# Kernel tuning notes

Hardware: AMD Instinct MI355X
Metric: run time of the kernel (lower is better)

The kernel has to match this reference:

```python
import jax, jax.numpy as jnp
import numpy as np

N_NODES = 100000
N_EDGES = 1280000
D_IN = 64
D_HID = 128
D_OUT = 64


def sage_conv(x, src, dst, W_l, b_l, W_r, n_nodes):
    # PyG SAGEConv (aggr='mean', root_weight=True):
    #   out_i = W_l @ mean_{j in N(i)} x_j + b_l + W_r @ x_i
    msg = x[src]  # [E, d] gather of source-node features
    agg = jax.ops.segment_sum(msg, dst, num_segments=n_nodes)  # [N, d]
    cnt = jax.ops.segment_sum(jnp.ones((src.shape[0], 1), x.dtype), dst,
                              num_segments=n_nodes)  # [N, 1]
    mean = agg / jnp.maximum(cnt, 1.0)  # zero-neighbor nodes -> 0 (matches scatter-mean)
    return mean @ W_l.T + b_l + x @ W_r.T


def setup_inputs() -> dict:
    key = jax.random.key(0)
    ks = jax.random.split(key, 8)
    x = jax.random.normal(ks[0], (N_NODES, D_IN), dtype=jnp.float32)
    edge_index = jax.random.randint(ks[1], (2, N_EDGES), 0, N_NODES, dtype=jnp.int64)
    s = 0.05
    W_l1 = jax.random.normal(ks[2], (D_HID, D_IN), dtype=jnp.float32) * s
    b_l1 = jnp.zeros((D_HID,), dtype=jnp.float32)
    W_r1 = jax.random.normal(ks[3], (D_HID, D_IN), dtype=jnp.float32) * s
    W_l2 = jax.random.normal(ks[4], (D_OUT, D_HID), dtype=jnp.float32) * s
    b_l2 = jnp.zeros((D_OUT,), dtype=jnp.float32)
    W_r2 = jax.random.normal(ks[5], (D_OUT, D_HID), dtype=jnp.float32) * s
    return {"x": x, "edge_index": edge_index,
            "W_l1": W_l1, "b_l1": b_l1, "W_r1": W_r1,
            "W_l2": W_l2, "b_l2": b_l2, "W_r2": W_r2}


def reference(x, edge_index, W_l1, b_l1, W_r1, W_l2, b_l2, W_r2):
    src, dst = edge_index[0], edge_index[1]
    n = x.shape[0]
    h = sage_conv(x, src, dst, W_l1, b_l1, W_r1, n)
    h = jax.nn.relu(h)
    out = sage_conv(h, src, dst, W_l2, b_l2, W_r2, n)
    return out
```

## Files before the change

### kernel.cpp

```cpp
#include <hip/hip_runtime.h>
#include <cstdint>
#include <cstddef>

typedef __attribute__((ext_vector_type(8))) short short8;
typedef __attribute__((ext_vector_type(4))) float floatx4;
typedef __attribute__((ext_vector_type(2))) float floatx2;
typedef __attribute__((ext_vector_type(4))) int intx4;

static constexpr int DIN  = 64;
static constexpr int DHID = 128;
static constexpr int BSH  = 7;
static constexpr int BNODES = 1 << BSH;
static constexpr int TILE = 8192;
static constexpr int CAP  = 4096;
static constexpr unsigned SENT = 0xFFFFFFFFu;

__device__ inline short f2bf(float f) {
  unsigned u = __float_as_uint(f);
  u += 0x7FFF + ((u >> 16) & 1);
  return (short)(u >> 16);
}
__device__ inline float bf2f(short s) {
  return __uint_as_float(((unsigned)(unsigned short)s) << 16);
}
__device__ inline floatx2 bfpair(unsigned u) {
  floatx2 r;
  r[0] = __uint_as_float(u << 16);
  r[1] = __uint_as_float(u & 0xFFFF0000u);
  return r;
}

__global__ __launch_bounds__(256) void part_prep_kernel(const void* edges, long long nmax,
    int* __restrict__ bucket_cursor, int* __restrict__ real_cnt,
    unsigned* __restrict__ packed, int E, int NB,
    const float* __restrict__ x,
    const float* __restrict__ Wl1, const float* __restrict__ Wr1,
    const float* __restrict__ Wl2, const float* __restrict__ Wr2,
    short* __restrict__ xb, short* __restrict__ wc1, short* __restrict__ wc2,
    int nx, int gP, int gx)
{
  __shared__ unsigned sval[TILE];
  __shared__ unsigned saux[TILE];
  __shared__ int hist[1024];
  __shared__ int gb[1024];
  __shared__ int smode;
  int t = threadIdx.x;
  int blk = blockIdx.x;
  if (blk >= gP) {
    int b = blk - gP;
    if (b < gx) {
      int i0 = (b * 256 + t) * 8;
      if (i0 < nx) {
        floatx4 f0 = *(const floatx4*)&x[i0];
        floatx4 f1 = *(const floatx4*)&x[i0 + 4];
        short8 o;
        o[0]=f2bf(f0[0]); o[1]=f2bf(f0[1]); o[2]=f2bf(f0[2]); o[3]=f2bf(f0[3]);
        o[4]=f2bf(f1[0]); o[5]=f2bf(f1[1]); o[6]=f2bf(f1[2]); o[7]=f2bf(f1[3]);
        *(short8*)&xb[i0] = o;
      }
    } else {
      int wb = b - gx;
      int idx = ((wb & 15) * 256 + t) * 4;
      int n = idx >> 7, k = idx & 127;
      const float* src;
      if (wb < 16) src = (k < 64) ? &Wl1[n * 64 + k] : &Wr1[n * 64 + (k - 64)];
      else         src = (n < 64) ? &Wl2[n * 128 + k] : &Wr2[(n - 64) * 128 + k];
      floatx4 f = *(const floatx4*)src;
      short* dst = (wb < 16 ? wc1 : wc2) + idx;
      dst[0]=f2bf(f[0]); dst[1]=f2bf(f[1]); dst[2]=f2bf(f[2]); dst[3]=f2bf(f[3]);
    }
    return;
  }
  int base = blk * TILE;
  int cnt_here = E - base; if (cnt_here > TILE) cnt_here = TILE;
  for (int i = t; i < NB; i += 256) hist[i] = 0;
  if (t == 0) smode = 1;
  __syncthreads();
  {
    const long long* e64 = (const long long*)edges;
    int nchk = E < 256 ? E : 256;
    bool ok = true;
    for (int i = t; i < nchk; i += 256) {
      long long v = e64[i];
      if (v < 0 || v >= nmax) ok = false;
    }
    if (!ok) smode = 0;
  }
  __syncthreads();
  bool m64 = (smode != 0);
  #pragma unroll 4
  for (int c = 0; c < TILE / 256; ++c) {
    int idx = c * 256 + t;
    if (idx < cnt_here) {
      int i = base + idx;
      int s, d;
      if (m64) { const long long* e = (const long long*)edges; s = (int)e[i]; d = (int)e[(size_t)E + i]; }
      else     { const int*       e = (const int*)edges;       s = e[i];      d = e[(size_t)E + i]; }
      int b = d >> BSH;
      int rank = atomicAdd(&hist[b], 1);
      sval[idx] = ((unsigned)(d & (BNODES - 1)) << 17) | (unsigned)s;
      saux[idx] = ((unsigned)b << 13) | (unsigned)rank;
    }
  }
  __syncthreads();
  for (int b = t; b < NB; b += 256) {
    int cnt = hist[b];
    int gbase = 0;
    if (cnt > 0) {
      int pad = (cnt + 15) & ~15;
      gbase = b * CAP + atomicAdd(&bucket_cursor[b], pad);
      atomicAdd(&real_cnt[b], cnt);
      for (int j = cnt; j < pad; ++j) packed[gbase + j] = SENT;
    }
    gb[b] = gbase;
  }
  __syncthreads();
  #pragma unroll 4
  for (int c = 0; c < TILE / 256; ++c) {
    int idx = c * 256 + t;
    if (idx < cnt_here) {
      unsigned a = saux[idx];
      packed[gb[a >> 13] + (a & 0x1FFFu)] = sval[idx];
    }
  }
}

__global__ __launch_bounds__(256) void bucket_sort_agg_kernel(const unsigned* __restrict__ packed,
    const int* __restrict__ bucket_cursor, const int* __restrict__ real_cnt,
    int* __restrict__ row_ptr, int* __restrict__ sorted_src,
    const short* __restrict__ feat, short* __restrict__ meanb, int N, int E) {
  __shared__ int nhist[BNODES];
  __shared__ int cur[BNODES];
  __shared__ int begs[BNODES];
  __shared__ int elist[CAP];
  __shared__ int wsum[4];
  __shared__ int redsum[4];
  int b = blockIdx.x, t = threadIdx.x;
  int partial = 0;
  for (int i = t; i < b; i += 256) partial += real_cnt[i];
  #pragma unroll
  for (int off = 1; off < 64; off <<= 1) partial += __shfl_xor(partial, off, 64);
  if ((t & 63) == 0) redsum[t >> 6] = partial;
  if (t < BNODES) nhist[t] = 0;
  if (b == 0 && t == 0) row_ptr[N] = E;
  __syncthreads();
  int eb = redsum[0] + redsum[1] + redsum[2] + redsum[3];
  int n0 = b << BSH;
  int nn = N - n0; if (nn > BNODES) nn = BNODES;
  int rbeg = b * CAP, rcnt = bucket_cursor[b];
  for (int i = t; i < rcnt; i += 256) {
    unsigned p = packed[rbeg + i];
    if (p != SENT) atomicAdd(&nhist[p >> 17], 1);
  }
  __syncthreads();
  int lane = t & 63, w = t >> 6;
  int v = (t < BNODES) ? nhist[t] : 0;
  int val = v;
  #pragma unroll
  for (int off = 1; off < 64; off <<= 1) {
    int u = __shfl_up(val, off, 64);
    if (lane >= off) val += u;
  }
  if (lane == 63) wsum[w] = val;
  __syncthreads();
  int pre = (w == 1) ? wsum[0] : 0;
  int excl = pre + val - v;
  if (t < nn) { row_ptr[n0 + t] = eb + excl; cur[t] = excl; begs[t] = excl; }
  __syncthreads();
  for (int i = t; i < rcnt; i += 256) {
    unsigned p = packed[rbeg + i];
    if (p != SENT) {
      int pos = atomicAdd(&cur[p >> 17], 1);
      int s = (int)(p & 0x1FFFFu);
      elist[pos] = s;
      sorted_src[eb + pos] = s;
    }
  }
  __syncthreads();
  int c = t & 7;
  const short* fbase = feat + c * 8;
  #pragma unroll
  for (int ch = 0; ch < 4; ++ch) {
    int ln = ch * 32 + (t >> 3);
    if (ln < nn) {
      int beg = begs[ln], end = cur[ln];
      floatx2 acc2[4];
      #pragma unroll
      for (int k = 0; k < 4; ++k) acc2[k] = (floatx2){0.f, 0.f};
      int e = beg;
      for (; e + 8 <= end; e += 8) {
        int s0 = elist[e],     s1 = elist[e + 1], s2 = elist[e + 2], s3 = elist[e + 3];
        int s4 = elist[e + 4], s5 = elist[e + 5], s6 = elist[e + 6], s7 = elist[e + 7];
        short8 v0 = *(const short8*)&fbase[(size_t)s0 * 64];
        short8 v1 = *(const short8*)&fbase[(size_t)s1 * 64];
        short8 v2 = *(const short8*)&fbase[(size_t)s2 * 64];
        short8 v3 = *(const short8*)&fbase[(size_t)s3 * 64];
        short8 v4 = *(const short8*)&fbase[(size_t)s4 * 64];
        short8 v5 = *(const short8*)&fbase[(size_t)s5 * 64];
        short8 v6 = *(const short8*)&fbase[(size_t)s6 * 64];
        short8 v7 = *(const short8*)&fbase[(size_t)s7 * 64];
        const unsigned* u0 = (const unsigned*)&v0;
        const unsigned* u1 = (const unsigned*)&v1;
        const unsigned* u2 = (const unsigned*)&v2;
        const unsigned* u3 = (const unsigned*)&v3;
        const unsigned* u4 = (const unsigned*)&v4;
        const unsigned* u5 = (const unsigned*)&v5;
        const unsigned* u6 = (const unsigned*)&v6;
        const unsigned* u7 = (const unsigned*)&v7;
        #pragma unroll
        for (int k = 0; k < 4; ++k) {
          floatx2 s01 = bfpair(u0[k]) + bfpair(u1[k]);
          floatx2 s23 = bfpair(u2[k]) + bfpair(u3[k]);
          floatx2 s45 = bfpair(u4[k]) + bfpair(u5[k]);
          floatx2 s67 = bfpair(u6[k]) + bfpair(u7[k]);
          acc2[k] += (s01 + s23) + (s45 + s67);
        }
      }
      for (; e < end; ++e) {
        short8 vv = *(const short8*)&fbase[(size_t)elist[e] * 64];
        const unsigned* uu = (const unsigned*)&vv;
        #pragma unroll
        for (int k = 0; k < 4; ++k) acc2[k] += bfpair(uu[k]);
      }
      float inv = 1.f / fmaxf((float)(end - beg), 1.f);
      short8 o;
      #pragma unroll
      for (int k = 0; k < 4; ++k) {
        o[2 * k]     = f2bf(acc2[k][0] * inv);
        o[2 * k + 1] = f2bf(acc2[k][1] * inv);
      }
      *(short8*)&meanb[(size_t)(n0 + ln) * 64 + c * 8] = o;
    }
  }
}

__global__ __launch_bounds__(256) void agg_epi_kernel(const short* __restrict__ feat,
                                                      const int* __restrict__ row_ptr,
                                                      const int* __restrict__ srcs,
                                                      const float* __restrict__ rbuf,
                                                      const float* __restrict__ bias,
                                                      float* __restrict__ outf, int N) {
  int node = blockIdx.x * 32 + (threadIdx.x >> 3);
  if (node >= N) return;
  int c = threadIdx.x & 7;
  const short* fbase = feat + c * 8;
  int beg = row_ptr[node], end = row_ptr[node + 1];
  floatx2 acc2[4];
  #pragma unroll
  for (int k = 0; k < 4; ++k) acc2[k] = (floatx2){0.f, 0.f};
  int e = beg;
  for (; e + 8 <= end; e += 8) {
    intx4 sa = *(const intx4*)&srcs[e];
    intx4 sb = *(const intx4*)&srcs[e + 4];
    short8 v0 = *(const short8*)&fbase[(size_t)sa[0] * 64];
    short8 v1 = *(const short8*)&fbase[(size_t)sa[1] * 64];
    short8 v2 = *(const short8*)&fbase[(size_t)sa[2] * 64];
    short8 v3 = *(const short8*)&fbase[(size_t)sa[3] * 64];
    short8 v4 = *(const short8*)&fbase[(size_t)sb[0] * 64];
    short8 v5 = *(const short8*)&fbase[(size_t)sb[1] * 64];
    short8 v6 = *(const short8*)&fbase[(size_t)sb[2] * 64];
    short8 v7 = *(const short8*)&fbase[(size_t)sb[3] * 64];
    const unsigned* u0 = (const unsigned*)&v0;
    const unsigned* u1 = (const unsigned*)&v1;
    const unsigned* u2 = (const unsigned*)&v2;
    const unsigned* u3 = (const unsigned*)&v3;
    const unsigned* u4 = (const unsigned*)&v4;
    const unsigned* u5 = (const unsigned*)&v5;
    const unsigned* u6 = (const unsigned*)&v6;
    const unsigned* u7 = (const unsigned*)&v7;
    #pragma unroll
    for (int k = 0; k < 4; ++k) {
      floatx2 s01 = bfpair(u0[k]) + bfpair(u1[k]);
      floatx2 s23 = bfpair(u2[k]) + bfpair(u3[k]);
      floatx2 s45 = bfpair(u4[k]) + bfpair(u5[k]);
      floatx2 s67 = bfpair(u6[k]) + bfpair(u7[k]);
      acc2[k] += (s01 + s23) + (s45 + s67);
    }
  }
  for (; e + 4 <= end; e += 4) {
    intx4 sa = *(const intx4*)&srcs[e];
    short8 v0 = *(const short8*)&fbase[(size_t)sa[0] * 64];
    short8 v1 = *(const short8*)&fbase[(size_t)sa[1] * 64];
    short8 v2 = *(const short8*)&fbase[(size_t)sa[2] * 64];
    short8 v3 = *(const short8*)&fbase[(size_t)sa[3] * 64];
    const unsigned* u0 = (const unsigned*)&v0;
    const unsigned* u1 = (const unsigned*)&v1;
    const unsigned* u2 = (const unsigned*)&v2;
    const unsigned* u3 = (const unsigned*)&v3;
    #pragma unroll
    for (int k = 0; k < 4; ++k) {
      floatx2 s01 = bfpair(u0[k]) + bfpair(u1[k]);
      floatx2 s23 = bfpair(u2[k]) + bfpair(u3[k]);
      acc2[k] += s01 + s23;
    }
  }
  for (; e < end; ++e) {
    short8 v = *(const short8*)&fbase[(size_t)srcs[e] * 64];
    const unsigned* u = (const unsigned*)&v;
    #pragma unroll
    for (int k = 0; k < 4; ++k) acc2[k] += bfpair(u[k]);
  }
  float acc[8];
  #pragma unroll
  for (int k = 0; k < 4; ++k) { acc[2 * k] = acc2[k][0]; acc[2 * k + 1] = acc2[k][1]; }
  float inv = 1.f / fmaxf((float)(end - beg), 1.f);
  floatx4 b0 = *(const floatx4*)&bias[c * 8];
  floatx4 b1 = *(const floatx4*)&bias[c * 8 + 4];
  floatx4 r0 = *(const floatx4*)&rbuf[(size_t)node * 64 + c * 8];
  floatx4 r1 = *(const floatx4*)&rbuf[(size_t)node * 64 + c * 8 + 4];
  floatx4 o0, o1;
  #pragma unroll
  for (int j = 0; j < 4; ++j) {
    o0[j] = acc[j] * inv + b0[j] + r0[j];
    o1[j] = acc[4 + j] * inv + b1[j] + r1[j];
  }
  *(floatx4*)&outf[(size_t)node * 64 + c * 8]     = o0;
  *(floatx4*)&outf[(size_t)node * 64 + c * 8 + 4] = o1;
}

__global__ __launch_bounds__(256) void fused_gemm_kernel(
    const short* __restrict__ Aa, const short* __restrict__ Ab,
    const short* __restrict__ wc1, const short* __restrict__ wc2,
    const float* __restrict__ bias1,
    short* __restrict__ Cg, float* __restrict__ Cr, int M)
{
  __shared__ short Ws[128][136];
  __shared__ short Hs[128][136];
  int t = threadIdx.x;
  #pragma unroll
  for (int i = 0; i < 8; ++i) {
    int idx = i * 256 + t;
    int r = idx >> 4, c8 = (idx & 15) * 8;
    *(short8*)&Ws[r][c8] = *(const short8*)&wc1[r * 128 + c8];
  }
  __syncthreads();
  int wv = t >> 6, lane = t & 63, q = lane >> 4, l15 = lane & 15;
  int m0 = blockIdx.x * 128 + wv * 32;
  floatx4 acc[2][8];
  #pragma unroll
  for (int mt = 0; mt < 2; ++mt)
    #pragma unroll
    for (int nt = 0; nt < 8; ++nt) acc[mt][nt] = (floatx4){0.f, 0.f, 0.f, 0.f};
  #pragma unroll
  for (int ko = 0; ko < 4; ++ko) {
    const short* Asrc = (ko < 2) ? Aa : Ab;
    short8 a[2];
    #pragma unroll
    for (int mt = 0; mt < 2; ++mt) {
      int row = m0 + mt * 16 + l15;
      a[mt] = (short8){0, 0, 0, 0, 0, 0, 0, 0};
      if (row < M) a[mt] = *(const short8*)&Asrc[(size_t)row * 64 + (ko & 1) * 32 + q * 8];
    }
    #pragma unroll
    for (int nt = 0; nt < 8; ++nt) {
      short8 bfr = *(const short8*)&Ws[nt * 16 + l15][ko * 32 + q * 8];
      acc[0][nt] = __builtin_amdgcn_mfma_f32_16x16x32_bf16(a[0], bfr, acc[0][nt], 0, 0, 0);
      acc[1][nt] = __builtin_amdgcn_mfma_f32_16x16x32_bf16(a[1], bfr, acc[1][nt], 0, 0, 0);
    }
  }
  #pragma unroll
  for (int mt = 0; mt < 2; ++mt) {
    #pragma unroll
    for (int nt = 0; nt < 8; ++nt) {
      int n = nt * 16 + l15;
      float bv = bias1[n];
      #pragma unroll
      for (int r2 = 0; r2 < 4; ++r2) {
        int lr = wv * 32 + mt * 16 + q * 4 + r2;
        float v = fmaxf(acc[mt][nt][r2] + bv, 0.f);
        Hs[lr][n] = f2bf(v);
      }
    }
  }
  __syncthreads();
  #pragma unroll
  for (int i = 0; i < 8; ++i) {
    int idx = i * 256 + t;
    int r = idx >> 4, c8 = (idx & 15) * 8;
    *(short8*)&Ws[r][c8] = *(const short8*)&wc2[r * 128 + c8];
  }
  __syncthreads();
  #pragma unroll
  for (int mt = 0; mt < 2; ++mt)
    #pragma unroll
    for (int nt = 0; nt < 8; ++nt) acc[mt][nt] = (floatx4){0.f, 0.f, 0.f, 0.f};
  #pragma unroll
  for (int ko = 0; ko < 4; ++ko) {
    short8 a[2];
    #pragma unroll
    for (int mt = 0; mt < 2; ++mt)
      a[mt] = *(const short8*)&Hs[wv * 32 + mt * 16 + l15][ko * 32 + q * 8];
    #pragma unroll
    for (int nt = 0; nt < 8; ++nt) {
      short8 bfr = *(const short8*)&Ws[nt * 16 + l15][ko * 32 + q * 8];
      acc[0][nt] = __builtin_amdgcn_mfma_f32_16x16x32_bf16(a[0], bfr, acc[0][nt], 0, 0, 0);
      acc[1][nt] = __builtin_amdgcn_mfma_f32_16x16x32_bf16(a[1], bfr, acc[1][nt], 0, 0, 0);
    }
  }
  #pragma unroll
  for (int mt = 0; mt < 2; ++mt) {
    #pragma unroll
    for (int nt = 0; nt < 8; ++nt) {
      int n = nt * 16 + l15;
      #pragma unroll
      for (int r2 = 0; r2 < 4; ++r2) {
        int mr = m0 + mt * 16 + q * 4 + r2;
        if (mr >= M) continue;
        float v = acc[mt][nt][r2];
        if (nt < 4) Cg[(size_t)mr * 64 + n] = f2bf(v);
        else        Cr[(size_t)mr * 64 + (n - 64)] = v;
      }
    }
  }
}

extern "C" void kernel_launch(void* const* d_in, const int* in_sizes, int n_in,
                              void* d_out, int out_size, void* d_ws, size_t ws_size,
                              hipStream_t stream) {
  const float* x   = (const float*)d_in[0];
  const void*  ei  = d_in[1];
  const float* Wl1 = (const float*)d_in[2];
  const float* bl1 = (const float*)d_in[3];
  const float* Wr1 = (const float*)d_in[4];
  const float* Wl2 = (const float*)d_in[5];
  const float* bl2 = (const float*)d_in[6];
  const float* Wr2 = (const float*)d_in[7];
  int N = in_sizes[0] / DIN;
  int E = in_sizes[1] / 2;
  int NB = (N + BNODES - 1) / BNODES;

  char* w = (char*)d_ws;
  size_t off = 0;
  auto alloc = [&](size_t bytes) -> void* {
    void* p = w + off;
    off += (bytes + 255) & ~(size_t)255;
    return p;
  };
  int*      bcur       = (int*)alloc((size_t)NB * 8);
  int*      rcnt       = bcur + NB;
  int*      row_ptr    = (int*)alloc(((size_t)N + 1) * 4);
  unsigned* packed     = (unsigned*)alloc((size_t)NB * CAP * 4);
  int*      sorted_src = (int*)alloc((size_t)E * 4);
  short*    xb         = (short*)alloc((size_t)N * 64 * 2);
  short*    meanb      = (short*)alloc((size_t)N * 64 * 2);
  float*    rbuf       = (float*)alloc((size_t)N * 64 * 4);
  short*    wc1        = (short*)alloc(128 * 128 * 2);
  short*    wc2        = (short*)alloc(128 * 128 * 2);
  (void)ws_size; (void)n_in; (void)out_size;

  hipMemsetAsync(bcur, 0, (size_t)NB * 8, stream);

  int nx = N * DIN;
  int gx = (nx / 8 + 255) / 256;
  int gP = (E + TILE - 1) / TILE;
  part_prep_kernel<<<gP + gx + 32, 256, 0, stream>>>(ei, (long long)N, bcur, rcnt, packed,
                                                     E, NB, x, Wl1, Wr1, Wl2, Wr2,
                                                     xb, wc1, wc2, nx, gP, gx);

  bucket_sort_agg_kernel<<<NB, 256, 0, stream>>>(packed, bcur, rcnt, row_ptr, sorted_src,
                                                 xb, meanb, N, E);

  int gm = (N + 127) / 128;
  fused_gemm_kernel<<<gm, 256, 0, stream>>>(meanb, xb, wc1, wc2, bl1, meanb, rbuf, N);

  int gN32 = (N + 31) / 32;
  agg_epi_kernel<<<gN32, 256, 0, stream>>>(meanb, row_ptr, sorted_src, rbuf, bl2, (float*)d_out, N);
}
```

Before: 201.1 us.

## Locally sort edges by bucket in LDS and drop sentinel padding

The partition kernel now computes a block-local exclusive scan of bucket counts, reorders edges into bucket-contiguous order in shared memory, and writes them out in a coalesced way. Slot reservation uses the exact count instead of padding to 16, so the sentinel fill, the separate real-count array and its atomics go away. The sort kernel reads bucket_cursor as the true count and no longer checks for sentinels. This trades an extra LDS pass and register arrays (32 values per thread) for fewer scattered global writes and less wasted bandwidth.

New measurement: 203.7 us. Within noise of the previous version (+1.3%).

```diff
diff --git a/kernel.cpp b/kernel.cpp
--- a/kernel.cpp
+++ b/kernel.cpp
@@ -13,7 +13,7 @@
 static constexpr int BNODES = 1 << BSH;
 static constexpr int TILE = 8192;
 static constexpr int CAP  = 4096;
-static constexpr unsigned SENT = 0xFFFFFFFFu;
+static constexpr int EPT  = TILE / 256;
 
 __device__ inline short f2bf(float f) {
   unsigned u = __float_as_uint(f);
@@ -31,7 +31,7 @@
 }
 
 __global__ __launch_bounds__(256) void part_prep_kernel(const void* edges, long long nmax,
-    int* __restrict__ bucket_cursor, int* __restrict__ real_cnt,
+    int* __restrict__ bucket_cursor,
     unsigned* __restrict__ packed, int E, int NB,
     const float* __restrict__ x,
     const float* __restrict__ Wl1, const float* __restrict__ Wr1,
@@ -39,10 +39,12 @@
     short* __restrict__ xb, short* __restrict__ wc1, short* __restrict__ wc2,
     int nx, int gP, int gx)
 {
-  __shared__ unsigned sval[TILE];
-  __shared__ unsigned saux[TILE];
+  __shared__ unsigned svals[TILE];
+  __shared__ unsigned short sbid[TILE];
   __shared__ int hist[1024];
+  __shared__ int lbase[1024];
   __shared__ int gb[1024];
+  __shared__ int wsum[4];
   __shared__ int smode;
   int t = threadIdx.x;
   int blk = blockIdx.x;
@@ -88,9 +90,12 @@
   }
   __syncthreads();
   bool m64 = (smode != 0);
-  #pragma unroll 4
-  for (int c = 0; c < TILE / 256; ++c) {
+  unsigned val[EPT];
+  unsigned aux[EPT];
+  #pragma unroll
+  for (int c = 0; c < EPT; ++c) {
     int idx = c * 256 + t;
+    val[c] = 0; aux[c] = 0;
     if (idx < cnt_here) {
       int i = base + idx;
       int s, d;
@@ -98,35 +103,64 @@
       else     { const int*       e = (const int*)edges;       s = e[i];      d = e[(size_t)E + i]; }
       int b = d >> BSH;
       int rank = atomicAdd(&hist[b], 1);
-      sval[idx] = ((unsigned)(d & (BNODES - 1)) << 17) | (unsigned)s;
-      saux[idx] = ((unsigned)b << 13) | (unsigned)rank;
-    }
-  }
-  __syncthreads();
-  for (int b = t; b < NB; b += 256) {
-    int cnt = hist[b];
-    int gbase = 0;
-    if (cnt > 0) {
-      int pad = (cnt + 15) & ~15;
-      gbase = b * CAP + atomicAdd(&bucket_cursor[b], pad);
-      atomicAdd(&real_cnt[b], cnt);
-      for (int j = cnt; j < pad; ++j) packed[gbase + j] = SENT;
-    }
-    gb[b] = gbase;
-  }
-  __syncthreads();
-  #pragma unroll 4
-  for (int c = 0; c < TILE / 256; ++c) {
+      val[c] = ((unsigned)(d & (BNODES - 1)) << 17) | (unsigned)s;
+      aux[c] = ((unsigned)b << 13) | (unsigned)rank;
+    }
+  }
+  __syncthreads();
+  {
+    int i0 = t * 4;
+    int v4[4]; int s = 0;
+    #pragma unroll
+    for (int c = 0; c < 4; ++c) { int idx = i0 + c; v4[c] = (idx < NB) ? hist[idx] : 0; s += v4[c]; }
+    int lane = t & 63, w = t >> 6;
+    int vv = s;
+    #pragma unroll
+    for (int off = 1; off < 64; off <<= 1) {
+      int u = __shfl_up(vv, off, 64);
+      if (lane >= off) vv += u;
+    }
+    if (lane == 63) wsum[w] = vv;
+    __syncthreads();
+    int wpre = 0;
+    for (int ww = 0; ww < w; ++ww) wpre += wsum[ww];
+    int run = wpre + vv - s;
+    #pragma unroll
+    for (int c = 0; c < 4; ++c) {
+      int idx = i0 + c;
+      if (idx < NB) {
+        int cnt = v4[c];
+        lbase[idx] = run;
+        gb[idx] = (cnt > 0) ? idx * CAP + atomicAdd(&bucket_cursor[idx], cnt) : 0;
+        run += cnt;
+      }
+    }
+  }
+  __syncthreads();
+  #pragma unroll
+  for (int c = 0; c < EPT; ++c) {
     int idx = c * 256 + t;
     if (idx < cnt_here) {
-      unsigned a = saux[idx];
-      packed[gb[a >> 13] + (a & 0x1FFFu)] = sval[idx];
+      int b = (int)(aux[c] >> 13);
+      int r = (int)(aux[c] & 0x1FFFu);
+      int p = lbase[b] + r;
+      svals[p] = val[c];
+      sbid[p] = (unsigned short)b;
+    }
+  }
+  __syncthreads();
+  #pragma unroll 4
+  for (int c = 0; c < EPT; ++c) {
+    int i = c * 256 + t;
+    if (i < cnt_here) {
+      int b = (int)sbid[i];
+      packed[gb[b] + (i - lbase[b])] = svals[i];
     }
   }
 }
 
 __global__ __launch_bounds__(256) void bucket_sort_agg_kernel(const unsigned* __restrict__ packed,
-    const int* __restrict__ bucket_cursor, const int* __restrict__ real_cnt,
+    const int* __restrict__ bucket_cursor,
     int* __restrict__ row_ptr, int* __restrict__ sorted_src,
     const short* __restrict__ feat, short* __restrict__ meanb, int N, int E) {
   __shared__ int nhist[BNODES];
@@ -137,7 +171,7 @@
   __shared__ int redsum[4];
   int b = blockIdx.x, t = threadIdx.x;
   int partial = 0;
-  for (int i = t; i < b; i += 256) partial += real_cnt[i];
+  for (int i = t; i < b; i += 256) partial += bucket_cursor[i];
   #pragma unroll
   for (int off = 1; off < 64; off <<= 1) partial += __shfl_xor(partial, off, 64);
   if ((t & 63) == 0) redsum[t >> 6] = partial;
@@ -150,7 +184,7 @@
   int rbeg = b * CAP, rcnt = bucket_cursor[b];
   for (int i = t; i < rcnt; i += 256) {
     unsigned p = packed[rbeg + i];
-    if (p != SENT) atomicAdd(&nhist[p >> 17], 1);
+    atomicAdd(&nhist[p >> 17], 1);
   }
   __syncthreads();
   int lane = t & 63, w = t >> 6;
@@ -169,12 +203,10 @@
   __syncthreads();
   for (int i = t; i < rcnt; i += 256) {
     unsigned p = packed[rbeg + i];
-    if (p != SENT) {
-      int pos = atomicAdd(&cur[p >> 17], 1);
-      int s = (int)(p & 0x1FFFFu);
-      elist[pos] = s;
-      sorted_src[eb + pos] = s;
-    }
+    int pos = atomicAdd(&cur[p >> 17], 1);
+    int s = (int)(p & 0x1FFFFu);
+    elist[pos] = s;
+    sorted_src[eb + pos] = s;
   }
   __syncthreads();
   int c = t & 7;
@@ -436,8 +468,7 @@
     off += (bytes + 255) & ~(size_t)255;
     return p;
   };
-  int*      bcur       = (int*)alloc((size_t)NB * 8);
-  int*      rcnt       = bcur + NB;
+  int*      bcur       = (int*)alloc((size_t)NB * 4);
   int*      row_ptr    = (int*)alloc(((size_t)N + 1) * 4);
   unsigned* packed     = (unsigned*)alloc((size_t)NB * CAP * 4);
   int*      sorted_src = (int*)alloc((size_t)E * 4);
@@ -448,16 +479,16 @@
   short*    wc2        = (short*)alloc(128 * 128 * 2);
   (void)ws_size; (void)n_in; (void)out_size;
 
-  hipMemsetAsync(bcur, 0, (size_t)NB * 8, stream);
+  hipMemsetAsync(bcur, 0, (size_t)NB * 4, stream);
 
   int nx = N * DIN;
   int gx = (nx / 8 + 255) / 256;
   int gP = (E + TILE - 1) / TILE;
-  part_prep_kernel<<<gP + gx + 32, 256, 0, stream>>>(ei, (long long)N, bcur, rcnt, packed,
+  part_prep_kernel<<<gP + gx + 32, 256, 0, stream>>>(ei, (long long)N, bcur, packed,
                                                      E, NB, x, Wl1, Wr1, Wl2, Wr2,
                                                      xb, wc1, wc2, nx, gP, gx);
 
-  bucket_sort_agg_kernel<<<NB, 256, 0, stream>>>(packed, bcur, rcnt, row_ptr, sorted_src,
+  bucket_sort_agg_kernel<<<NB, 256, 0, stream>>>(packed, bcur, row_ptr, sorted_src,
                                                  xb, meanb, N, E);
 
   int gm = (N + 127) / 128;
```
